# Kernel optimization log

Hardware: AMD Instinct MI355X
Metric: run time of the kernel (lower is better)

## Reference

```python
import jax, jax.numpy as jnp
import numpy as np
from jax import lax

B_, K_, T_, V_ = 2, 4, 1024, 1024
D_MODEL, EXPAND = 512, 2
D_INNER = EXPAND * D_MODEL          # 1024
N_STATE, D_CONV, DT_RANK, L_ = 16, 4, 32, 2


def setup_inputs() -> dict:
    key = jax.random.key(0)
    ks = jax.random.split(key, 9)
    s = 0.02
    A0 = jnp.log(jnp.arange(1, N_STATE + 1, dtype=jnp.float32))  # S4D-real init
    return {
        'codes': jax.random.randint(ks[0], (B_, K_, T_), 0, V_),
        'embed_w': jax.random.normal(ks[1], (K_, V_, D_MODEL), jnp.float32) * s,
        'norm_w': jnp.ones((L_, D_MODEL), jnp.float32),
        'in_proj_w': jax.random.normal(ks[2], (L_, 2 * D_INNER, D_MODEL), jnp.float32) * s,
        'conv_w': jax.random.normal(ks[3], (L_, D_INNER, 1, D_CONV), jnp.float32) * s,
        'conv_b': jnp.zeros((L_, D_INNER), jnp.float32),
        'x_proj_w': jax.random.normal(ks[4], (L_, DT_RANK + 2 * N_STATE, D_INNER), jnp.float32) * s,
        'dt_proj_w': jax.random.normal(ks[5], (L_, D_INNER, DT_RANK), jnp.float32) * s,
        'dt_proj_b': jnp.zeros((L_, D_INNER), jnp.float32),
        'A_log': jnp.broadcast_to(A0, (L_, D_INNER, N_STATE)) + 0.0,
        'D_skip': jnp.ones((L_, D_INNER), jnp.float32),
        'out_proj_w': jax.random.normal(ks[6], (L_, D_MODEL, D_INNER), jnp.float32) * s,
        'head_w': jax.random.normal(ks[7], (K_, D_MODEL, V_), jnp.float32) * s,
    }


def rmsnorm(x, w, eps=1e-6):
    return x * w * lax.rsqrt(jnp.mean(x * x, axis=-1, keepdims=True) + eps)


def causal_dwconv(x, w, b):
    # x: (B,T,D); w: (D,1,d_conv) depthwise; torch pads d_conv-1 both sides then slices [:T]
    # == left-pad-only causal conv.
    xt = x.transpose(0, 2, 1)  # (B,D,T)
    y = lax.conv_general_dilated(xt, w, (1,), [(D_CONV - 1, 0)],
                                 feature_group_count=D_INNER,
                                 dimension_numbers=('NCH', 'OIH', 'NCH'))
    return (y + b[None, :, None]).transpose(0, 2, 1)


def mamba_block(x, norm_w, in_w, cw, cb, xp_w, dtp_w, dtp_b, A_log, D_skip, out_w):
    res = x
    x = rmsnorm(x, norm_w)
    xz = x @ in_w.T                                   # (B,T,2*d_inner)
    x_ssm, z = jnp.split(xz, 2, axis=-1)
    x_ssm = jax.nn.silu(causal_dwconv(x_ssm, cw, cb))  # (B,T,D)
    x_dbl = x_ssm @ xp_w.T                            # (B,T,dt_rank+2N)
    dt_lr, Bm, Cm = jnp.split(x_dbl, [DT_RANK, DT_RANK + N_STATE], axis=-1)
    dt = jax.nn.softplus(dt_lr @ dtp_w.T + dtp_b)     # (B,T,D)
    A = -jnp.exp(A_log)                               # (D,N)
    dA = jnp.exp(dt[..., None] * A)                   # (B,T,D,N)
    dBx = dt[..., None] * Bm[:, :, None, :] * x_ssm[..., None]  # (B,T,D,N)

    def step(h, inp):
        dA_t, dBx_t, C_t = inp
        h = dA_t * h + dBx_t                          # (B,D,N)
        return h, jnp.einsum('bdn,bn->bd', h, C_t)

    h0 = jnp.zeros((x.shape[0], D_INNER, N_STATE), x.dtype)
    _, ys = lax.scan(step, h0, (dA.transpose(1, 0, 2, 3),
                                dBx.transpose(1, 0, 2, 3),
                                Cm.transpose(1, 0, 2)))
    y = ys.transpose(1, 0, 2) + x_ssm * D_skip        # (B,T,D)
    y = y * jax.nn.silu(z)
    return res + y @ out_w.T


def reference(codes, embed_w, norm_w, in_proj_w, conv_w, conv_b, x_proj_w,
              dt_proj_w, dt_proj_b, A_log, D_skip, out_proj_w, head_w):
    k_idx = jnp.arange(K_)[None, :, None]
    x = embed_w[k_idx, codes].sum(axis=1)             # (B,T,d_model): RVQ sum-embedding
    for l in range(L_):
        x = mamba_block(x, norm_w[l], in_proj_w[l], conv_w[l], conv_b[l],
                        x_proj_w[l], dt_proj_w[l], dt_proj_b[l],
                        A_log[l], D_skip[l], out_proj_w[l])
    return jnp.einsum('btd,kdv->bktv', x, head_w)     # (B,K,T,V)
```

## Files before the change

kernel.cpp:

```cpp
#include <hip/hip_runtime.h>
#include <hip/hip_bf16.h>


#define B_SZ 2
#define K_CB 4
#define T_SZ 1024
#define V_SZ 1024
#define DM 512
#define DI 1024
#define NS 16
#define DTR 32
#define NCHUNK 64
#define TCHUNK 16

typedef unsigned short u16;
typedef long long ll;
using short8 = __attribute__((ext_vector_type(8))) short;
using f32x4  = __attribute__((ext_vector_type(4))) float;

__device__ __forceinline__ float bf2f(u16 u) {
    union { unsigned int i; float f; } v; v.i = ((unsigned int)u) << 16; return v.f;
}
__device__ __forceinline__ u16 f2bf(float f) {
    union { float f; unsigned int i; } v; v.f = f;
    unsigned int x = v.i;
    return (u16)((x + 0x7fffu + ((x >> 16) & 1u)) >> 16);
}
__device__ __forceinline__ float siluf(float x) { return x / (1.f + __expf(-x)); }
__device__ __forceinline__ float softplusf(float x) { return (x > 20.f) ? x : log1pf(__expf(x)); }

__global__ __launch_bounds__(256) void wcvt_k(const float* __restrict__ a, u16* __restrict__ da, int na,
                                              const float* __restrict__ b2, u16* __restrict__ db, int nb,
                                              const float* __restrict__ c, u16* __restrict__ dc, int nc,
                                              const float* __restrict__ d, u16* __restrict__ dd) {
    int i = blockIdx.x * 256 + threadIdx.x;
    if (i < na) { da[i] = f2bf(a[i]); return; }
    i -= na;
    if (i < nb) { db[i] = f2bf(b2[i]); return; }
    i -= nb;
    if (i < nc) { dc[i] = f2bf(c[i]); return; }
    i -= nc;
    dd[i] = f2bf(d[i]);
}

__global__ __launch_bounds__(256) void ht_k(const float* __restrict__ w, u16* __restrict__ wt) {
    __shared__ float tile[64][65];
    int z = blockIdx.z;
    int v0 = blockIdx.x << 6, d0 = blockIdx.y << 6;
    int col = threadIdx.x & 63, rbase = threadIdx.x >> 6;
#pragma unroll
    for (int i = 0; i < 16; i++) {
        int row = (i << 2) + rbase;
        tile[row][col] = w[(ll)z * (DM * V_SZ) + (ll)(d0 + row) * V_SZ + v0 + col];
    }
    __syncthreads();
#pragma unroll
    for (int i = 0; i < 16; i++) {
        int vrow = (i << 2) + rbase;
        wt[(ll)z * (V_SZ * DM) + (ll)(v0 + vrow) * DM + d0 + col] = f2bf(tile[col][vrow]);
    }
}

__global__ __launch_bounds__(256) void cvt_k(const float* __restrict__ s, u16* __restrict__ d) {
    int i = blockIdx.x * 256 + threadIdx.x;
    d[i] = f2bf(s[i]);
}

__global__ __launch_bounds__(512) void embed_k(const int* __restrict__ codes,
                                               const float* __restrict__ ew,
                                               float* __restrict__ x) {
    int row = blockIdx.x;
    int b = row >> 10, t = row & 1023;
    int d = threadIdx.x;
    float acc = 0.f;
#pragma unroll
    for (int k = 0; k < K_CB; k++) {
        int c = codes[b * (K_CB * T_SZ) + k * T_SZ + t];
        acc += ew[((ll)k * V_SZ + c) * DM + d];
    }
    x[(ll)row * DM + d] = acc;
}

__global__ __launch_bounds__(256) void rmsnorm_k(const float* __restrict__ x,
                                                 const float* __restrict__ w,
                                                 u16* __restrict__ xn) {
    ll row = blockIdx.x;
    const float* xr = x + row * DM;
    int tid = threadIdx.x;
    float v0 = xr[tid], v1 = xr[tid + 256];
    float ss = v0 * v0 + v1 * v1;
#pragma unroll
    for (int off = 32; off > 0; off >>= 1) ss += __shfl_down(ss, off, 64);
    __shared__ float red[4];
    if ((tid & 63) == 0) red[tid >> 6] = ss;
    __syncthreads();
    float tot = red[0] + red[1] + red[2] + red[3];
    float scale = rsqrtf(tot * (1.0f / DM) + 1e-6f);
    xn[row * DM + tid]       = f2bf(v0 * scale * w[tid]);
    xn[row * DM + tid + 256] = f2bf(v1 * scale * w[tid + 256]);
}

template <int EP>
__global__ __launch_bounds__(256) void mgemm_k(const u16* __restrict__ A, int lda,
                                               const u16* __restrict__ W,
                                               float* __restrict__ C, int ldc, int K,
                                               const float* __restrict__ bias,
                                               u16* __restrict__ Cb, int ldcb) {
    __shared__ u16 As[64][40];
    __shared__ u16 Bs[64][40];
    int tid = threadIdx.x;
    int m0 = blockIdx.y << 6, n0 = blockIdx.x << 6;
    if (EP == 4) W += (ll)blockIdx.z * (V_SZ * DM);
    int lane = tid & 63, wave = tid >> 6;
    int q = lane >> 4, r = lane & 15;
    int wm = (wave >> 1) << 5, wn = (wave & 1) << 5;
    int srow = tid >> 2, sseg = (tid & 3) << 3;
    f32x4 acc[2][2];
#pragma unroll
    for (int i = 0; i < 2; i++)
#pragma unroll
        for (int j = 0; j < 2; j++) acc[i][j] = (f32x4){0.f, 0.f, 0.f, 0.f};

    for (int k0 = 0; k0 < K; k0 += 32) {
        *(uint4*)&As[srow][sseg] = *(const uint4*)&A[(ll)(m0 + srow) * lda + k0 + sseg];
        *(uint4*)&Bs[srow][sseg] = *(const uint4*)&W[(ll)(n0 + srow) * K + k0 + sseg];
        __syncthreads();
        short8 af[2], bfr[2];
#pragma unroll
        for (int i = 0; i < 2; i++) af[i]  = *(const short8*)&As[wm + (i << 4) + r][q << 3];
#pragma unroll
        for (int j = 0; j < 2; j++) bfr[j] = *(const short8*)&Bs[wn + (j << 4) + r][q << 3];
#pragma unroll
        for (int i = 0; i < 2; i++)
#pragma unroll
            for (int j = 0; j < 2; j++)
                acc[i][j] = __builtin_amdgcn_mfma_f32_16x16x32_bf16(af[i], bfr[j], acc[i][j], 0, 0, 0);
        __syncthreads();
    }

#pragma unroll
    for (int i = 0; i < 2; i++)
#pragma unroll
        for (int j = 0; j < 2; j++)
#pragma unroll
            for (int g = 0; g < 4; g++) {
                int m = m0 + wm + (i << 4) + (q << 2) + g;
                int n = n0 + wn + (j << 4) + r;
                float v = acc[i][j][g];
                if (EP == 0) {
                    Cb[(ll)m * ldcb + n] = f2bf(v);
                } else if (EP == 1) {
                    C[(ll)m * ldc + n] = v;
                } else if (EP == 2) {
                    C[(ll)m * ldc + n] = softplusf(v + bias[n]);
                } else if (EP == 3) {
                    float nv = C[(ll)m * ldc + n] + v;
                    C[(ll)m * ldc + n] = nv;
                    Cb[(ll)m * ldcb + n] = f2bf(nv);
                } else {
                    int b = m >> 10, t = m & 1023;
                    C[(ll)b * (K_CB * (ll)T_SZ * V_SZ) + (ll)blockIdx.z * (T_SZ * V_SZ)
                      + (ll)t * V_SZ + n] = v;
                }
            }
}

__global__ __launch_bounds__(256) void conv_k(const u16* __restrict__ xzb,
                                              const float* __restrict__ cw,
                                              const float* __restrict__ cb,
                                              float* __restrict__ xc,
                                              u16* __restrict__ xcb) {
    int row = blockIdx.x;
    int b = row >> 10, t = row & 1023;
    for (int c = threadIdx.x; c < DI; c += 256) {
        float acc = cb[c];
#pragma unroll
        for (int j = 0; j < 4; j++) {
            int tt = t - 3 + j;
            if (tt >= 0)
                acc += bf2f(xzb[((ll)(b * T_SZ + tt)) * (2 * DI) + c]) * cw[c * 4 + j];
        }
        float s = siluf(acc);
        xc[(ll)row * DI + c] = s;
        xcb[(ll)row * DI + c] = f2bf(s);
    }
}

__global__ __launch_bounds__(256) void scan1_k(const float* __restrict__ dt,
                                               const float* __restrict__ xc,
                                               const float* __restrict__ xdbl,
                                               const float* __restrict__ A_log,
                                               float* __restrict__ pA, float* __restrict__ U) {
    int blk = blockIdx.x;
    int dblk = blk & 3;
    int c = (blk >> 2) & (NCHUNK - 1);
    int b = blk >> 8;
    int d = dblk * 256 + threadIdx.x;
    float Av[NS];
#pragma unroll
    for (int n = 0; n < NS; n++) Av[n] = -__expf(A_log[d * NS + n]);
    float p[NS], u[NS];
#pragma unroll
    for (int n = 0; n < NS; n++) { p[n] = 1.f; u[n] = 0.f; }
    int t0 = c * TCHUNK;
    for (int s = 0; s < TCHUNK; s++) {
        ll ro = (ll)b * T_SZ + t0 + s;
        float dtv = dt[ro * DI + d];
        float xv = xc[ro * DI + d];
        float dx = dtv * xv;
        const float* Brow = xdbl + ro * 64 + DTR;
#pragma unroll
        for (int n = 0; n < NS; n++) {
            float a = __expf(dtv * Av[n]);
            p[n] *= a;
            u[n] = fmaf(a, u[n], dx * Brow[n]);
        }
    }
    ll o = (((ll)b * NCHUNK + c) * DI + d) * NS;
#pragma unroll
    for (int n = 0; n < NS; n++) { pA[o + n] = p[n]; U[o + n] = u[n]; }
}

__global__ __launch_bounds__(256) void scan2_k(const float* __restrict__ pA,
                                               const float* __restrict__ U,
                                               float* __restrict__ hst) {
    int i = blockIdx.x * 256 + threadIdx.x;
    int b = i >> 14;
    int rest = i & 16383;
    float h = 0.f;
#pragma unroll
    for (int c = 0; c < NCHUNK; c++) {
        ll o = ((ll)b * NCHUNK + c) * (DI * NS) + rest;
        float pa = pA[o], u = U[o];
        hst[o] = h;
        h = fmaf(pa, h, u);
    }
}

__global__ __launch_bounds__(256) void scan3_k(const float* __restrict__ dt,
                                               const float* __restrict__ xc,
                                               const float* __restrict__ xdbl,
                                               const u16* __restrict__ xzb,
                                               const float* __restrict__ A_log,
                                               const float* __restrict__ Dk,
                                               const float* __restrict__ hst,
                                               u16* __restrict__ y) {
    int blk = blockIdx.x;
    int dblk = blk & 3;
    int c = (blk >> 2) & (NCHUNK - 1);
    int b = blk >> 8;
    int d = dblk * 256 + threadIdx.x;
    float Av[NS];
#pragma unroll
    for (int n = 0; n < NS; n++) Av[n] = -__expf(A_log[d * NS + n]);
    float h[NS];
    ll ho = (((ll)b * NCHUNK + c) * DI + d) * NS;
#pragma unroll
    for (int n = 0; n < NS; n++) h[n] = hst[ho + n];
    float Dv = Dk[d];
    int t0 = c * TCHUNK;
    for (int s = 0; s < TCHUNK; s++) {
        ll ro = (ll)b * T_SZ + t0 + s;
        float dtv = dt[ro * DI + d];
        float xv = xc[ro * DI + d];
        float dx = dtv * xv;
        const float* Brow = xdbl + ro * 64 + DTR;
        const float* Crow = xdbl + ro * 64 + DTR + NS;
        float acc = 0.f;
#pragma unroll
        for (int n = 0; n < NS; n++) {
            float a = __expf(dtv * Av[n]);
            h[n] = fmaf(a, h[n], dx * Brow[n]);
            acc = fmaf(h[n], Crow[n], acc);
        }
        float zv = bf2f(xzb[ro * (2 * DI) + DI + d]);
        y[ro * DI + d] = f2bf((acc + xv * Dv) * siluf(zv));
    }
}

extern "C" void kernel_launch(void* const* d_in, const int* in_sizes, int n_in,
                              void* d_out, int out_size, void* d_ws, size_t ws_size,
                              hipStream_t stream) {
    const int*   codes   = (const int*)d_in[0];
    const float* embed_w = (const float*)d_in[1];
    const float* norm_w  = (const float*)d_in[2];
    const float* in_w    = (const float*)d_in[3];
    const float* conv_w  = (const float*)d_in[4];
    const float* conv_b  = (const float*)d_in[5];
    const float* xp_w    = (const float*)d_in[6];
    const float* dtp_w   = (const float*)d_in[7];
    const float* dtp_b   = (const float*)d_in[8];
    const float* A_log   = (const float*)d_in[9];
    const float* D_skip  = (const float*)d_in[10];
    const float* out_w   = (const float*)d_in[11];
    const float* head_w  = (const float*)d_in[12];
    float* out = (float*)d_out;

    float* ws = (float*)d_ws;
    float* x    = ws;
    float* xc   = x + 1048576;
    float* dtb  = xc + 2097152;
    float* xdbl = dtb + 2097152;
    float* pA   = xdbl + 131072;
    float* Uh   = pA + 2097152;

    u16* us       = (u16*)(Uh + 2097152);
    u16* xz_bf    = us;
    u16* xc_bf    = xz_bf + 4194304;
    u16* ybxn_bf  = xc_bf + 2097152;
    u16* xdbl_bf  = ybxn_bf + 2097152;
    u16* w_in_bf  = xdbl_bf + 131072;
    u16* w_xp_bf  = w_in_bf + 2097152;
    u16* w_dt_bf  = w_xp_bf + 131072;
    u16* w_out_bf = w_dt_bf + 65536;
    u16* w_hd_bf  = w_out_bf + 1048576;

    u16* xn_bf = ybxn_bf;
    u16* y_bf  = ybxn_bf;
    u16* x_bf  = xc_bf;

    const int M = B_SZ * T_SZ;

    wcvt_k<<<13056, 256, 0, stream>>>(in_w, w_in_bf, 2097152,
                                      xp_w, w_xp_bf, 131072,
                                      dtp_w, w_dt_bf, 65536,
                                      out_w, w_out_bf);
    ht_k<<<dim3(16, 8, 4), 256, 0, stream>>>(head_w, w_hd_bf);

    embed_k<<<M, 512, 0, stream>>>(codes, embed_w, x);

    for (int l = 0; l < 2; l++) {
        const float* al = A_log + l * DI * NS;
        rmsnorm_k<<<M, 256, 0, stream>>>(x, norm_w + l * DM, xn_bf);
        mgemm_k<0><<<dim3(32, 32), 256, 0, stream>>>(xn_bf, DM, w_in_bf + l * 1048576,
                                                     nullptr, 0, DM, nullptr, xz_bf, 2 * DI);
        conv_k<<<M, 256, 0, stream>>>(xz_bf, conv_w + l * DI * 4, conv_b + l * DI, xc, xc_bf);
        mgemm_k<1><<<dim3(1, 32), 256, 0, stream>>>(xc_bf, DI, w_xp_bf + l * 65536,
                                                    xdbl, 64, DI, nullptr, nullptr, 0);
        cvt_k<<<512, 256, 0, stream>>>(xdbl, xdbl_bf);
        mgemm_k<2><<<dim3(16, 32), 256, 0, stream>>>(xdbl_bf, 64, w_dt_bf + l * 32768,
                                                     dtb, DI, DTR, dtp_b + l * DI, nullptr, 0);
        scan1_k<<<512, 256, 0, stream>>>(dtb, xc, xdbl, al, pA, Uh);
        scan2_k<<<128, 256, 0, stream>>>(pA, Uh, Uh);
        scan3_k<<<512, 256, 0, stream>>>(dtb, xc, xdbl, xz_bf, al, D_skip + l * DI, Uh, y_bf);
        mgemm_k<3><<<dim3(8, 32), 256, 0, stream>>>(y_bf, DI, w_out_bf + l * 524288,
                                                    x, DM, DI, nullptr, x_bf, DM);
    }

    mgemm_k<4><<<dim3(16, 32, 4), 256, 0, stream>>>(x_bf, DM, w_hd_bf,
                                                    out, 0, DM, nullptr, nullptr, 0);
}
```

Baseline: 349.0 us.

## Add 128x128 global-to-LDS GEMM, fuse embed+rmsnorm, vectorize conv, scan, and converts

Adds a new 128x128-tile MFMA GEMM that loads tiles directly into LDS via global_load_lds and uses it for the in_proj and head projections. Fuses the embedding sum with the first RMSNorm, folds the xdbl bf16 conversion into the x_proj GEMM epilogue, vectorizes the weight conversion and depthwise conv to 4-wide accesses, and stages the B/C rows in shared memory for the scan kernels. These aim to cut launches, global traffic and per-tile overhead. The large tiles mean fewer blocks (256 for in_proj), which may lower occupancy, and the unpadded LDS layout may cause bank conflicts.

After: 334.0 us. 1.04x faster.

```diff
diff --git a/kernel.cpp b/kernel.cpp
--- a/kernel.cpp
+++ b/kernel.cpp
@@ -29,18 +29,33 @@
 __device__ __forceinline__ float siluf(float x) { return x / (1.f + __expf(-x)); }
 __device__ __forceinline__ float softplusf(float x) { return (x > 20.f) ? x : log1pf(__expf(x)); }
 
-__global__ __launch_bounds__(256) void wcvt_k(const float* __restrict__ a, u16* __restrict__ da, int na,
-                                              const float* __restrict__ b2, u16* __restrict__ db, int nb,
-                                              const float* __restrict__ c, u16* __restrict__ dc, int nc,
-                                              const float* __restrict__ d, u16* __restrict__ dd) {
-    int i = blockIdx.x * 256 + threadIdx.x;
-    if (i < na) { da[i] = f2bf(a[i]); return; }
-    i -= na;
-    if (i < nb) { db[i] = f2bf(b2[i]); return; }
-    i -= nb;
-    if (i < nc) { dc[i] = f2bf(c[i]); return; }
-    i -= nc;
-    dd[i] = f2bf(d[i]);
+__device__ __forceinline__ void gld16(const void* g, void* l) {
+    __builtin_amdgcn_global_load_lds(
+        (const __attribute__((address_space(1))) unsigned int*)g,
+        (__attribute__((address_space(3))) unsigned int*)l, 16, 0, 0);
+}
+
+__global__ __launch_bounds__(256) void wcvt4_k(const float* __restrict__ in_w,
+                                               const float* __restrict__ xp_w,
+                                               const float* __restrict__ dtp_w,
+                                               const float* __restrict__ out_w,
+                                               u16* __restrict__ w_in, u16* __restrict__ w_xp,
+                                               u16* __restrict__ w_dt, u16* __restrict__ w_out) {
+    int i = (blockIdx.x * 256 + threadIdx.x) << 2;
+    const float* s; u16* d;
+    if (i < 2097152) { s = in_w + i; d = w_in + i; }
+    else {
+        i -= 2097152;
+        if (i < 131072) { s = xp_w + i; d = w_xp + i; }
+        else {
+            i -= 131072;
+            if (i < 65536) { s = dtp_w + i; d = w_dt + i; }
+            else { i -= 65536; s = out_w + i; d = w_out + i; }
+        }
+    }
+    float4 v = *(const float4*)s;
+    ushort4 o; o.x = f2bf(v.x); o.y = f2bf(v.y); o.z = f2bf(v.z); o.w = f2bf(v.w);
+    *(ushort4*)d = o;
 }
 
 __global__ __launch_bounds__(256) void ht_k(const float* __restrict__ w, u16* __restrict__ wt) {
@@ -61,14 +76,11 @@
     }
 }
 
-__global__ __launch_bounds__(256) void cvt_k(const float* __restrict__ s, u16* __restrict__ d) {
-    int i = blockIdx.x * 256 + threadIdx.x;
-    d[i] = f2bf(s[i]);
-}
-
-__global__ __launch_bounds__(512) void embed_k(const int* __restrict__ codes,
-                                               const float* __restrict__ ew,
-                                               float* __restrict__ x) {
+__global__ __launch_bounds__(512) void embrms_k(const int* __restrict__ codes,
+                                                const float* __restrict__ ew,
+                                                const float* __restrict__ nw,
+                                                float* __restrict__ x,
+                                                u16* __restrict__ xn) {
     int row = blockIdx.x;
     int b = row >> 10, t = row & 1023;
     int d = threadIdx.x;
@@ -79,6 +91,15 @@
         acc += ew[((ll)k * V_SZ + c) * DM + d];
     }
     x[(ll)row * DM + d] = acc;
+    float ss = acc * acc;
+#pragma unroll
+    for (int off = 32; off > 0; off >>= 1) ss += __shfl_down(ss, off, 64);
+    __shared__ float red[8];
+    if ((d & 63) == 0) red[d >> 6] = ss;
+    __syncthreads();
+    float tot = red[0] + red[1] + red[2] + red[3] + red[4] + red[5] + red[6] + red[7];
+    float scale = rsqrtf(tot * (1.0f / DM) + 1e-6f);
+    xn[(ll)row * DM + d] = f2bf(acc * scale * nw[d]);
 }
 
 __global__ __launch_bounds__(256) void rmsnorm_k(const float* __restrict__ x,
@@ -98,6 +119,65 @@
     float scale = rsqrtf(tot * (1.0f / DM) + 1e-6f);
     xn[row * DM + tid]       = f2bf(v0 * scale * w[tid]);
     xn[row * DM + tid + 256] = f2bf(v1 * scale * w[tid + 256]);
+}
+
+template <int EP>
+__global__ __launch_bounds__(256) void mgemm2_k(const u16* __restrict__ A, int lda,
+                                                const u16* __restrict__ W,
+                                                float* __restrict__ C,
+                                                u16* __restrict__ Cb, int ldcb, int K) {
+    __shared__ u16 As[4096];
+    __shared__ u16 Bs[4096];
+    int tid = threadIdx.x;
+    int wave = tid >> 6, lane = tid & 63;
+    int q = lane >> 4, r = lane & 15;
+    int m0 = blockIdx.y << 7, n0 = blockIdx.x << 7;
+    const u16* Wz = W;
+    if (EP == 4) Wz += (ll)blockIdx.z * ((ll)V_SZ * DM);
+    int wm = (wave >> 1) << 6, wn = (wave & 1) << 6;
+    int sa0 = (wave << 7) + lane, sa1 = sa0 + 64;
+    f32x4 acc[4][4];
+#pragma unroll
+    for (int i = 0; i < 4; i++)
+#pragma unroll
+        for (int j = 0; j < 4; j++) acc[i][j] = (f32x4){0.f, 0.f, 0.f, 0.f};
+
+    for (int k0 = 0; k0 < K; k0 += 32) {
+        gld16(A  + (ll)(m0 + (sa0 >> 2)) * lda + k0 + ((sa0 & 3) << 3), &As[wave << 10]);
+        gld16(A  + (ll)(m0 + (sa1 >> 2)) * lda + k0 + ((sa1 & 3) << 3), &As[(wave << 10) + 512]);
+        gld16(Wz + (ll)(n0 + (sa0 >> 2)) * K   + k0 + ((sa0 & 3) << 3), &Bs[wave << 10]);
+        gld16(Wz + (ll)(n0 + (sa1 >> 2)) * K   + k0 + ((sa1 & 3) << 3), &Bs[(wave << 10) + 512]);
+        __syncthreads();
+        short8 af[4], bfr[4];
+#pragma unroll
+        for (int i = 0; i < 4; i++) af[i]  = *(const short8*)&As[((wm + (i << 4) + r) << 5) + (q << 3)];
+#pragma unroll
+        for (int j = 0; j < 4; j++) bfr[j] = *(const short8*)&Bs[((wn + (j << 4) + r) << 5) + (q << 3)];
+#pragma unroll
+        for (int i = 0; i < 4; i++)
+#pragma unroll
+            for (int j = 0; j < 4; j++)
+                acc[i][j] = __builtin_amdgcn_mfma_f32_16x16x32_bf16(af[i], bfr[j], acc[i][j], 0, 0, 0);
+        __syncthreads();
+    }
+
+#pragma unroll
+    for (int i = 0; i < 4; i++)
+#pragma unroll
+        for (int j = 0; j < 4; j++)
+#pragma unroll
+            for (int g = 0; g < 4; g++) {
+                int m = m0 + wm + (i << 4) + (q << 2) + g;
+                int n = n0 + wn + (j << 4) + r;
+                float v = acc[i][j][g];
+                if (EP == 0) {
+                    Cb[(ll)m * ldcb + n] = f2bf(v);
+                } else {
+                    int b = m >> 10, t = m & 1023;
+                    C[(ll)b * (K_CB * (ll)T_SZ * V_SZ) + (ll)blockIdx.z * (T_SZ * V_SZ)
+                      + (ll)t * V_SZ + n] = v;
+                }
+            }
 }
 
 template <int EP>
@@ -110,7 +190,6 @@
     __shared__ u16 Bs[64][40];
     int tid = threadIdx.x;
     int m0 = blockIdx.y << 6, n0 = blockIdx.x << 6;
-    if (EP == 4) W += (ll)blockIdx.z * (V_SZ * DM);
     int lane = tid & 63, wave = tid >> 6;
     int q = lane >> 4, r = lane & 15;
     int wm = (wave >> 1) << 5, wn = (wave & 1) << 5;
@@ -147,20 +226,15 @@
                 int m = m0 + wm + (i << 4) + (q << 2) + g;
                 int n = n0 + wn + (j << 4) + r;
                 float v = acc[i][j][g];
-                if (EP == 0) {
+                if (EP == 1) {
+                    C[(ll)m * ldc + n] = v;
                     Cb[(ll)m * ldcb + n] = f2bf(v);
-                } else if (EP == 1) {
-                    C[(ll)m * ldc + n] = v;
                 } else if (EP == 2) {
                     C[(ll)m * ldc + n] = softplusf(v + bias[n]);
-                } else if (EP == 3) {
+                } else {
                     float nv = C[(ll)m * ldc + n] + v;
                     C[(ll)m * ldc + n] = nv;
                     Cb[(ll)m * ldcb + n] = f2bf(nv);
-                } else {
-                    int b = m >> 10, t = m & 1023;
-                    C[(ll)b * (K_CB * (ll)T_SZ * V_SZ) + (ll)blockIdx.z * (T_SZ * V_SZ)
-                      + (ll)t * V_SZ + n] = v;
                 }
             }
 }
@@ -172,18 +246,28 @@
                                               u16* __restrict__ xcb) {
     int row = blockIdx.x;
     int b = row >> 10, t = row & 1023;
-    for (int c = threadIdx.x; c < DI; c += 256) {
-        float acc = cb[c];
-#pragma unroll
-        for (int j = 0; j < 4; j++) {
-            int tt = t - 3 + j;
-            if (tt >= 0)
-                acc += bf2f(xzb[((ll)(b * T_SZ + tt)) * (2 * DI) + c]) * cw[c * 4 + j];
+    int c0 = threadIdx.x << 2;
+    float4 a = *(const float4*)&cb[c0];
+    float acc[4] = {a.x, a.y, a.z, a.w};
+    float4 cwv[4];
+#pragma unroll
+    for (int e = 0; e < 4; e++) cwv[e] = *(const float4*)&cw[(c0 + e) << 2];
+#pragma unroll
+    for (int j = 0; j < 4; j++) {
+        int tt = t - 3 + j;
+        if (tt >= 0) {
+            ushort4 v = *(const ushort4*)&xzb[((ll)(b * T_SZ + tt)) * (2 * DI) + c0];
+            acc[0] = fmaf(bf2f(v.x), ((const float*)&cwv[0])[j], acc[0]);
+            acc[1] = fmaf(bf2f(v.y), ((const float*)&cwv[1])[j], acc[1]);
+            acc[2] = fmaf(bf2f(v.z), ((const float*)&cwv[2])[j], acc[2]);
+            acc[3] = fmaf(bf2f(v.w), ((const float*)&cwv[3])[j], acc[3]);
         }
-        float s = siluf(acc);
-        xc[(ll)row * DI + c] = s;
-        xcb[(ll)row * DI + c] = f2bf(s);
-    }
+    }
+    float4 s; ushort4 sb;
+    s.x = siluf(acc[0]); s.y = siluf(acc[1]); s.z = siluf(acc[2]); s.w = siluf(acc[3]);
+    sb.x = f2bf(s.x); sb.y = f2bf(s.y); sb.z = f2bf(s.z); sb.w = f2bf(s.w);
+    *(float4*)&xc[(ll)row * DI + c0] = s;
+    *(ushort4*)&xcb[(ll)row * DI + c0] = sb;
 }
 
 __global__ __launch_bounds__(256) void scan1_k(const float* __restrict__ dt,
@@ -196,24 +280,34 @@
     int c = (blk >> 2) & (NCHUNK - 1);
     int b = blk >> 8;
     int d = dblk * 256 + threadIdx.x;
+    int t0 = c * TCHUNK;
+    __shared__ float BC[TCHUNK][32];
+    if (threadIdx.x < TCHUNK * 8) {
+        int rr = threadIdx.x >> 3, cc = (threadIdx.x & 7) << 2;
+        *(float4*)&BC[rr][cc] = *(const float4*)&xdbl[((ll)(b * T_SZ + t0 + rr)) * 64 + DTR + cc];
+    }
     float Av[NS];
 #pragma unroll
-    for (int n = 0; n < NS; n++) Av[n] = -__expf(A_log[d * NS + n]);
+    for (int n4 = 0; n4 < 4; n4++) {
+        float4 alv = *(const float4*)&A_log[d * NS + (n4 << 2)];
+        Av[(n4 << 2) + 0] = -__expf(alv.x); Av[(n4 << 2) + 1] = -__expf(alv.y);
+        Av[(n4 << 2) + 2] = -__expf(alv.z); Av[(n4 << 2) + 3] = -__expf(alv.w);
+    }
+    __syncthreads();
     float p[NS], u[NS];
 #pragma unroll
     for (int n = 0; n < NS; n++) { p[n] = 1.f; u[n] = 0.f; }
-    int t0 = c * TCHUNK;
+#pragma unroll
     for (int s = 0; s < TCHUNK; s++) {
-        ll ro = (ll)b * T_SZ + t0 + s;
+        ll ro = (ll)(b * T_SZ + t0 + s);
         float dtv = dt[ro * DI + d];
         float xv = xc[ro * DI + d];
         float dx = dtv * xv;
-        const float* Brow = xdbl + ro * 64 + DTR;
 #pragma unroll
         for (int n = 0; n < NS; n++) {
             float a = __expf(dtv * Av[n]);
             p[n] *= a;
-            u[n] = fmaf(a, u[n], dx * Brow[n]);
+            u[n] = fmaf(a, u[n], dx * BC[s][n]);
         }
     }
     ll o = (((ll)b * NCHUNK + c) * DI + d) * NS;
@@ -250,28 +344,37 @@
     int c = (blk >> 2) & (NCHUNK - 1);
     int b = blk >> 8;
     int d = dblk * 256 + threadIdx.x;
+    int t0 = c * TCHUNK;
+    __shared__ float BC[TCHUNK][32];
+    if (threadIdx.x < TCHUNK * 8) {
+        int rr = threadIdx.x >> 3, cc = (threadIdx.x & 7) << 2;
+        *(float4*)&BC[rr][cc] = *(const float4*)&xdbl[((ll)(b * T_SZ + t0 + rr)) * 64 + DTR + cc];
+    }
     float Av[NS];
 #pragma unroll
-    for (int n = 0; n < NS; n++) Av[n] = -__expf(A_log[d * NS + n]);
+    for (int n4 = 0; n4 < 4; n4++) {
+        float4 alv = *(const float4*)&A_log[d * NS + (n4 << 2)];
+        Av[(n4 << 2) + 0] = -__expf(alv.x); Av[(n4 << 2) + 1] = -__expf(alv.y);
+        Av[(n4 << 2) + 2] = -__expf(alv.z); Av[(n4 << 2) + 3] = -__expf(alv.w);
+    }
     float h[NS];
     ll ho = (((ll)b * NCHUNK + c) * DI + d) * NS;
 #pragma unroll
     for (int n = 0; n < NS; n++) h[n] = hst[ho + n];
     float Dv = Dk[d];
-    int t0 = c * TCHUNK;
+    __syncthreads();
+#pragma unroll
     for (int s = 0; s < TCHUNK; s++) {
-        ll ro = (ll)b * T_SZ + t0 + s;
+        ll ro = (ll)(b * T_SZ + t0 + s);
         float dtv = dt[ro * DI + d];
         float xv = xc[ro * DI + d];
         float dx = dtv * xv;
-        const float* Brow = xdbl + ro * 64 + DTR;
-        const float* Crow = xdbl + ro * 64 + DTR + NS;
         float acc = 0.f;
 #pragma unroll
         for (int n = 0; n < NS; n++) {
             float a = __expf(dtv * Av[n]);
-            h[n] = fmaf(a, h[n], dx * Brow[n]);
-            acc = fmaf(h[n], Crow[n], acc);
+            h[n] = fmaf(a, h[n], dx * BC[s][n]);
+            acc = fmaf(h[n], BC[s][16 + n], acc);
         }
         float zv = bf2f(xzb[ro * (2 * DI) + DI + d]);
         y[ro * DI + d] = f2bf((acc + xv * Dv) * siluf(zv));
@@ -321,23 +424,21 @@
 
     const int M = B_SZ * T_SZ;
 
-    wcvt_k<<<13056, 256, 0, stream>>>(in_w, w_in_bf, 2097152,
-                                      xp_w, w_xp_bf, 131072,
-                                      dtp_w, w_dt_bf, 65536,
-                                      out_w, w_out_bf);
+    wcvt4_k<<<3264, 256, 0, stream>>>(in_w, xp_w, dtp_w, out_w,
+                                      w_in_bf, w_xp_bf, w_dt_bf, w_out_bf);
     ht_k<<<dim3(16, 8, 4), 256, 0, stream>>>(head_w, w_hd_bf);
 
-    embed_k<<<M, 512, 0, stream>>>(codes, embed_w, x);
+    embrms_k<<<M, 512, 0, stream>>>(codes, embed_w, norm_w, x, xn_bf);
 
     for (int l = 0; l < 2; l++) {
         const float* al = A_log + l * DI * NS;
-        rmsnorm_k<<<M, 256, 0, stream>>>(x, norm_w + l * DM, xn_bf);
-        mgemm_k<0><<<dim3(32, 32), 256, 0, stream>>>(xn_bf, DM, w_in_bf + l * 1048576,
-                                                     nullptr, 0, DM, nullptr, xz_bf, 2 * DI);
+        if (l == 1)
+            rmsnorm_k<<<M, 256, 0, stream>>>(x, norm_w + DM, xn_bf);
+        mgemm2_k<0><<<dim3(16, 16), 256, 0, stream>>>(xn_bf, DM, w_in_bf + l * 1048576,
+                                                      nullptr, xz_bf, 2 * DI, DM);
         conv_k<<<M, 256, 0, stream>>>(xz_bf, conv_w + l * DI * 4, conv_b + l * DI, xc, xc_bf);
         mgemm_k<1><<<dim3(1, 32), 256, 0, stream>>>(xc_bf, DI, w_xp_bf + l * 65536,
-                                                    xdbl, 64, DI, nullptr, nullptr, 0);
-        cvt_k<<<512, 256, 0, stream>>>(xdbl, xdbl_bf);
+                                                    xdbl, 64, DI, nullptr, xdbl_bf, 64);
         mgemm_k<2><<<dim3(16, 32), 256, 0, stream>>>(xdbl_bf, 64, w_dt_bf + l * 32768,
                                                      dtb, DI, DTR, dtp_b + l * DI, nullptr, 0);
         scan1_k<<<512, 256, 0, stream>>>(dtb, xc, xdbl, al, pA, Uh);
@@ -347,6 +448,6 @@
                                                     x, DM, DI, nullptr, x_bf, DM);
     }
 
-    mgemm_k<4><<<dim3(16, 32, 4), 256, 0, stream>>>(x_bf, DM, w_hd_bf,
-                                                    out, 0, DM, nullptr, nullptr, 0);
-}
+    mgemm2_k<4><<<dim3(8, 16, 4), 256, 0, stream>>>(x_bf, DM, w_hd_bf,
+                                                    out, nullptr, 0, DM);
+}
```
